# Kernel tuning notes

Measured on AMD Instinct MI355X. Metric: run time of the kernel, lower is better.

The kernel has to match this reference:

```python
import jax, jax.numpy as jnp
import numpy as np

NUM_HEADS = 8
NUM_GROUPS = 32
EPS = 1e-5


def group_norm(x, gamma, beta):
    b, c, h, w = x.shape
    xg = x.reshape(b, NUM_GROUPS, c // NUM_GROUPS, h, w)
    mean = jnp.mean(xg, axis=(2, 3, 4), keepdims=True)
    var = jnp.var(xg, axis=(2, 3, 4), keepdims=True)
    xn = ((xg - mean) * jax.lax.rsqrt(var + EPS)).reshape(b, c, h, w)
    return xn * gamma[None, :, None, None] + beta[None, :, None, None]


def setup_inputs() -> dict:
    key = jax.random.key(0)
    ks = jax.random.split(key, 4)
    b, c, h, w = 16, 512, 32, 32
    x = jax.random.normal(ks[0], (b, c, h, w), dtype=jnp.float32)
    gn_gamma = jnp.ones((c,), dtype=jnp.float32)
    gn_beta = jnp.zeros((c,), dtype=jnp.float32)
    qkv_w = jax.random.normal(ks[1], (3 * c, c), dtype=jnp.float32) * (1.0 / np.sqrt(c))
    qkv_b = jnp.zeros((3 * c,), dtype=jnp.float32)
    proj_w = jax.random.normal(ks[2], (c, c), dtype=jnp.float32) * (1.0 / np.sqrt(c))
    proj_b = jnp.zeros((c,), dtype=jnp.float32)
    return {"x": x, "gn_gamma": gn_gamma, "gn_beta": gn_beta,
            "qkv_w": qkv_w, "qkv_b": qkv_b, "proj_w": proj_w, "proj_b": proj_b}


def reference(x, gn_gamma, gn_beta, qkv_w, qkv_b, proj_w, proj_b):
    b, c, h, w = x.shape
    hd = c // NUM_HEADS
    hw = h * w

    xn = group_norm(x, gn_gamma, gn_beta)
    # 1x1 conv == channel matmul
    qkv = jnp.einsum('oc,bchw->bohw', qkv_w, xn) + qkv_b[None, :, None, None]
    q, k, v = jnp.split(qkv, 3, axis=1)
    q = q.reshape(b, NUM_HEADS, hd, hw)
    k = k.reshape(b, NUM_HEADS, hd, hw)
    v = v.reshape(b, NUM_HEADS, hd, hw)

    scale = 1.0 / np.sqrt(hd)
    attn = jnp.einsum('bhdt,bhds->bhts', q, k) * scale  # [b,H,hw,hw]
    attn = jax.nn.softmax(attn, axis=-1)
    h_attn = jnp.einsum('bhts,bhds->bhdt', attn, v).reshape(b, c, h, w)

    h_attn = jnp.einsum('oc,bchw->bohw', proj_w, h_attn) + proj_b[None, :, None, None]
    return x + h_attn
```

## Files before the change

kernel.cpp:

```cpp
#include <hip/hip_runtime.h>
#include <math.h>

#define NUM_HEADS 8
#define NUM_GROUPS 32
#define EPS 1e-5f

constexpr int B  = 16;
constexpr int C  = 512;
constexpr int HW = 1024;
constexpr int HD = 64;

typedef short bf16x8 __attribute__((ext_vector_type(8)));
typedef float f32x4  __attribute__((ext_vector_type(4)));

#define QSCALE 0.1803368801111f

__device__ inline unsigned short f2bf(float f) {
    union { float f; unsigned int u; } v; v.f = f;
    unsigned int r = (v.u + 0x7FFFu + ((v.u >> 16) & 1u)) >> 16;
    return (unsigned short)r;
}

__device__ __forceinline__ unsigned int pack_trunc(float lo, float hi) {
    return __builtin_amdgcn_perm(__float_as_uint(hi), __float_as_uint(lo), 0x07060302u);
}

__device__ __forceinline__ void gld_lds16(void* lds, const void* g) {
    __builtin_amdgcn_global_load_lds(
        (const __attribute__((address_space(1))) void*)g,
        (__attribute__((address_space(3))) void*)lds, 16, 0, 0);
}

__global__ __launch_bounds__(256)
void groupnorm_t_kernel(const float* __restrict__ x,
                        const float* __restrict__ gamma,
                        const float* __restrict__ beta,
                        unsigned short* __restrict__ xnT) {
    const int bg = blockIdx.x;
    const int b = bg >> 5, g = bg & 31;
    const size_t base = ((size_t)b * C + (size_t)g * 16) * HW;

    float v[4][16];
    float sum = 0.f, sumsq = 0.f;
    #pragma unroll
    for (int p = 0; p < 4; ++p) {
        const int t = threadIdx.x + p * 256;
        #pragma unroll
        for (int cl = 0; cl < 16; ++cl) {
            const float f = x[base + (size_t)cl * HW + t];
            v[p][cl] = f;
            sum += f;
            sumsq += f * f;
        }
    }
    #pragma unroll
    for (int off = 32; off > 0; off >>= 1) {
        sum   += __shfl_down(sum, off, 64);
        sumsq += __shfl_down(sumsq, off, 64);
    }
    __shared__ float s_sum[4], s_sq[4];
    const int wid = threadIdx.x >> 6, lane = threadIdx.x & 63;
    if (lane == 0) { s_sum[wid] = sum; s_sq[wid] = sumsq; }
    __syncthreads();
    const float tsum = s_sum[0] + s_sum[1] + s_sum[2] + s_sum[3];
    const float tsq  = s_sq[0] + s_sq[1] + s_sq[2] + s_sq[3];
    const float mean = tsum * (1.0f / 16384.f);
    const float var  = tsq * (1.0f / 16384.f) - mean * mean;
    const float rstd = rsqrtf(var + EPS);

    float ga[16], be[16];
    #pragma unroll
    for (int cl = 0; cl < 16; ++cl) {
        ga[cl] = gamma[g * 16 + cl] * rstd;
        be[cl] = beta[g * 16 + cl] - mean * ga[cl];
    }

    #pragma unroll
    for (int p = 0; p < 4; ++p) {
        const int t = threadIdx.x + p * 256;
        unsigned short pk[16];
        #pragma unroll
        for (int cl = 0; cl < 16; ++cl)
            pk[cl] = f2bf(v[p][cl] * ga[cl] + be[cl]);
        unsigned short* dst = xnT + ((size_t)(b * 1024 + t)) * 512 + g * 16;
        *(uint4*)dst = *(const uint4*)pk;
        *(uint4*)(dst + 8) = *(const uint4*)(pk + 8);
    }
}

__global__ __launch_bounds__(256)
void wconv_kernel(const float* __restrict__ qkv_w,
                  const float* __restrict__ proj_w,
                  unsigned short* __restrict__ wqb) {
    const int i = blockIdx.x * 256 + threadIdx.x;
    const int n1 = 786432 / 4;
    const int nt = 1048576 / 4;
    if (i >= nt) return;
    const float4 v = (i < n1) ? ((const float4*)qkv_w)[i]
                              : ((const float4*)proj_w)[i - n1];
    ushort4 r;
    r.x = f2bf(v.x); r.y = f2bf(v.y); r.z = f2bf(v.z); r.w = f2bf(v.w);
    ((ushort4*)wqb)[i] = r;
}

__device__ __forceinline__ void mfma_gemm_core(const char* __restrict__ Ab,
                                               const char* __restrict__ Bb,
                                               unsigned short* As,
                                               unsigned short* Bs,
                                               f32x4 acc[4][4]) {
    const int tid = threadIdx.x;
    const int w = tid >> 6, lane = tid & 63;
    const int lo = lane & 15, q4 = lane >> 4;
    const int wm = w >> 1, wn = w & 1;
    const int lrow = lane >> 2, lkc = lane & 3;

    for (int k0 = 0; k0 < 512; k0 += 32) {
        __syncthreads();
        #pragma unroll
        for (int i = 0; i < 2; ++i) {
            const int row = w * 32 + i * 16 + lrow;
            const int kc = lkc ^ ((row >> 1) & 3);
            const size_t goff = (size_t)row * 1024 + k0 * 2 + kc * 16;
            gld_lds16((char*)As + w * 2048 + i * 1024, Ab + goff);
            gld_lds16((char*)Bs + w * 2048 + i * 1024, Bb + goff);
        }
        __syncthreads();

        bf16x8 af[4], bfr[4];
        #pragma unroll
        for (int i = 0; i < 4; ++i) {
            const int ra = wm * 64 + i * 16 + lo;
            af[i]  = *(const bf16x8*)(As + ra * 32 + (q4 ^ ((ra >> 1) & 3)) * 8);
            const int rb = wn * 64 + i * 16 + lo;
            bfr[i] = *(const bf16x8*)(Bs + rb * 32 + (q4 ^ ((rb >> 1) & 3)) * 8);
        }
        #pragma unroll
        for (int mi = 0; mi < 4; ++mi)
            #pragma unroll
            for (int ni = 0; ni < 4; ++ni)
                acc[mi][ni] = __builtin_amdgcn_mfma_f32_16x16x32_bf16(
                    af[mi], bfr[ni], acc[mi][ni], 0, 0, 0);
    }
}

__global__ __launch_bounds__(256)
void qkv_mfma_kernel(const unsigned short* __restrict__ wqb,
                     const unsigned short* __restrict__ xnT,
                     const float* __restrict__ qkv_b,
                     unsigned short* __restrict__ Qt,
                     unsigned short* __restrict__ Kt,
                     unsigned short* __restrict__ Vb) {
    __shared__ __align__(16) unsigned short SMEM[8192];
    unsigned short* As = SMEM;
    unsigned short* Bs = SMEM + 4096;
    const int batch = blockIdx.z;
    const int mBase = blockIdx.y * 128, nBase = blockIdx.x * 128;

    f32x4 acc[4][4] = {};
    mfma_gemm_core((const char*)(wqb + (size_t)mBase * 512),
                   (const char*)(xnT + ((size_t)batch * 1024 + nBase) * 512),
                   As, Bs, acc);

    const int tid = threadIdx.x;
    const int w = tid >> 6, lane = tid & 63;
    const int lo = lane & 15, q4 = lane >> 4;
    const int wm = w >> 1, wn = w & 1;
    const int mw = mBase + wm * 64;
    const int tb = nBase + wn * 64;

    __syncthreads();

    if (mw < 1024) {
        const bool isQ = mw < 512;
        const int head = (mw >> 6) & 7;
        unsigned short* dst = (isQ ? Qt : Kt) + (((size_t)batch * 8 + head) << 16);
        const float sc = isQ ? QSCALE : 1.0f;
        #pragma unroll
        for (int mi = 0; mi < 4; ++mi) {
            const float4 bq = *(const float4*)(qkv_b + mw + mi * 16 + q4 * 4);
            #pragma unroll
            for (int ni = 0; ni < 4; ++ni) {
                const int t = tb + ni * 16 + lo;
                ushort4 pk;
                pk.x = f2bf((acc[mi][ni][0] + bq.x) * sc);
                pk.y = f2bf((acc[mi][ni][1] + bq.y) * sc);
                pk.z = f2bf((acc[mi][ni][2] + bq.z) * sc);
                pk.w = f2bf((acc[mi][ni][3] + bq.w) * sc);
                *(ushort4*)(dst + (size_t)t * 64 + mi * 16 + q4 * 4) = pk;
            }
        }
    } else {
        unsigned short* T = SMEM + w * 2048;
        unsigned short* Vrow = Vb + (size_t)batch * 524288 + (size_t)(mw - 1024) * 1024 + tb;
        const int rl8 = lane >> 3, c8 = lane & 7;
        #pragma unroll
        for (int p = 0; p < 2; ++p) {
            #pragma unroll
            for (int mi2 = 0; mi2 < 2; ++mi2) {
                const int mi = 2 * p + mi2;
                const float4 bq = *(const float4*)(qkv_b + mw + mi * 16 + q4 * 4);
                const int dl = mi2 * 16 + q4 * 4;
                #pragma unroll
                for (int ni = 0; ni < 4; ++ni) {
                    const int tl = ni * 16 + lo;
                    T[(dl + 0) * 64 + tl] = f2bf(acc[mi][ni][0] + bq.x);
                    T[(dl + 1) * 64 + tl] = f2bf(acc[mi][ni][1] + bq.y);
                    T[(dl + 2) * 64 + tl] = f2bf(acc[mi][ni][2] + bq.z);
                    T[(dl + 3) * 64 + tl] = f2bf(acc[mi][ni][3] + bq.w);
                }
            }
            #pragma unroll
            for (int i = 0; i < 4; ++i) {
                const int dl = i * 8 + rl8;
                const uint4 val = *(const uint4*)&T[dl * 64 + c8 * 8];
                *(uint4*)(Vrow + (size_t)(p * 32 + dl) * 1024 + c8 * 8) = val;
            }
        }
    }
}

__global__ __launch_bounds__(256, 4)
void attn_mfma_kernel(const unsigned short* __restrict__ Qt,
                      const unsigned short* __restrict__ Kt,
                      const unsigned short* __restrict__ Vb,
                      unsigned short* __restrict__ attnT) {
    const int bh = blockIdx.x;
    const int b = bh >> 3, h = bh & 7;
    const int tBase = blockIdx.y * 128;
    const int tid = threadIdx.x;
    const int w = tid >> 6, lane = tid & 63;
    const int lo = lane & 15, q4 = lane >> 4;
    const int xr = lo & 7;

    __shared__ __align__(16) unsigned short Ks[64 * 64];
    __shared__ __align__(16) unsigned short Vs[64 * 64];
    __shared__ __align__(16) unsigned short Ps[4 * 2048];

    const unsigned short* Kp = Kt + ((size_t)bh << 16);
    const unsigned short* Vp = Vb + ((size_t)b * 512 + h * 64) * 1024;

    bf16x8 qf[2][2];
    {
        const unsigned short* Qp = Qt + ((size_t)bh * 1024 + tBase + 32 * w) * 64;
        #pragma unroll
        for (int nt = 0; nt < 2; ++nt) {
            qf[nt][0] = *(const bf16x8*)(Qp + (size_t)(16 * nt + lo) * 64 + 8 * q4);
            qf[nt][1] = *(const bf16x8*)(Qp + (size_t)(16 * nt + lo) * 64 + 32 + 8 * q4);
        }
    }

    const int rl = lane >> 3, p8 = lane & 7;
    auto stage = [&](int s0) {
        #pragma unroll
        for (int cc = 0; cc < 2; ++cc) {
            const int r = 16 * w + 8 * cc + rl;
            const int jj = p8 ^ (r & 7);
            gld_lds16(Ks + (16 * w + 8 * cc) * 64, Kp + (size_t)(s0 + r) * 64 + jj * 8);
            gld_lds16(Vs + (16 * w + 8 * cc) * 64, Vp + (size_t)r * 1024 + s0 + jj * 8);
        }
    };

    f32x4 oacc[4][2] = {};
    float lrun[2] = {0.f, 0.f};
    unsigned short* Pw = Ps + w * 2048;

    for (int i = 0; i < 16; ++i) {
        if (i) __syncthreads();
        stage(i * 64);
        __syncthreads();

        f32x4 sacc[4][2] = {};
        #pragma unroll
        for (int mt = 0; mt < 4; ++mt) {
            const unsigned short* kr = Ks + (16 * mt + lo) * 64;
            const bf16x8 a0 = *(const bf16x8*)(kr + ((q4    ) ^ xr) * 8);
            const bf16x8 a1 = *(const bf16x8*)(kr + ((q4 + 4) ^ xr) * 8);
            #pragma unroll
            for (int nt = 0; nt < 2; ++nt) {
                sacc[mt][nt] = __builtin_amdgcn_mfma_f32_16x16x32_bf16(a0, qf[nt][0], sacc[mt][nt], 0, 0, 0);
                sacc[mt][nt] = __builtin_amdgcn_mfma_f32_16x16x32_bf16(a1, qf[nt][1], sacc[mt][nt], 0, 0, 0);
            }
        }

        #pragma unroll
        for (int nt = 0; nt < 2; ++nt) {
            const int t = 16 * nt + lo;
            float ps = 0.f;
            #pragma unroll
            for (int mt = 0; mt < 4; ++mt) {
                const f32x4 s = sacc[mt][nt];
                const float p0 = exp2f(s[0]);
                const float p1 = exp2f(s[1]);
                const float p2 = exp2f(s[2]);
                const float p3 = exp2f(s[3]);
                ps += (p0 + p1) + (p2 + p3);
                uint2 pk;
                pk.x = pack_trunc(p0, p1);
                pk.y = pack_trunc(p2, p3);
                const int sc = 2 * mt + (q4 >> 1);
                *(uint2*)(Pw + t * 64 + ((sc ^ xr) * 8) + 4 * (q4 & 1)) = pk;
            }
            lrun[nt] += ps;
        }

        bf16x8 bp[2][2];
        #pragma unroll
        for (int nt = 0; nt < 2; ++nt) {
            const unsigned short* pr = Pw + (16 * nt + lo) * 64;
            bp[nt][0] = *(const bf16x8*)(pr + ((q4    ) ^ xr) * 8);
            bp[nt][1] = *(const bf16x8*)(pr + ((q4 + 4) ^ xr) * 8);
        }
        #pragma unroll
        for (int md = 0; md < 4; ++md) {
            const unsigned short* vr = Vs + (16 * md + lo) * 64;
            const bf16x8 v0 = *(const bf16x8*)(vr + ((q4    ) ^ xr) * 8);
            const bf16x8 v1 = *(const bf16x8*)(vr + ((q4 + 4) ^ xr) * 8);
            #pragma unroll
            for (int nt = 0; nt < 2; ++nt) {
                oacc[md][nt] = __builtin_amdgcn_mfma_f32_16x16x32_bf16(v0, bp[nt][0], oacc[md][nt], 0, 0, 0);
                oacc[md][nt] = __builtin_amdgcn_mfma_f32_16x16x32_bf16(v1, bp[nt][1], oacc[md][nt], 0, 0, 0);
            }
        }
    }

    #pragma unroll
    for (int nt = 0; nt < 2; ++nt) {
        float lt = lrun[nt];
        lt += __shfl_xor(lt, 16, 64);
        lt += __shfl_xor(lt, 32, 64);
        const float inv = 1.0f / lt;
        const int t = tBase + 32 * w + 16 * nt + lo;
        unsigned short* op = attnT + ((size_t)(b * 1024 + t)) * 512 + h * 64;
        #pragma unroll
        for (int md = 0; md < 4; ++md) {
            uint2 pk;
            pk.x = pack_trunc(oacc[md][nt][0] * inv, oacc[md][nt][1] * inv);
            pk.y = pack_trunc(oacc[md][nt][2] * inv, oacc[md][nt][3] * inv);
            *(uint2*)(op + 16 * md + 4 * q4) = pk;
        }
    }
}

__global__ __launch_bounds__(256)
void proj_mfma_kernel(const unsigned short* __restrict__ wpb,
                      const unsigned short* __restrict__ attnT,
                      const float* __restrict__ proj_b,
                      const float* __restrict__ x,
                      float* __restrict__ out) {
    __shared__ __align__(16) unsigned short As[128 * 32];
    __shared__ __align__(16) unsigned short Bs[128 * 32];
    const int batch = blockIdx.z;
    const int mBase = blockIdx.y * 128, nBase = blockIdx.x * 128;

    f32x4 acc[4][4] = {};
    mfma_gemm_core((const char*)(wpb + (size_t)mBase * 512),
                   (const char*)(attnT + ((size_t)batch * 1024 + nBase) * 512),
                   As, Bs, acc);

    const int tid = threadIdx.x;
    const int w = tid >> 6, lane = tid & 63;
    const int lo = lane & 15, q4 = lane >> 4;
    const int wm = w >> 1, wn = w & 1;
    const float* xb = x + (size_t)batch * 524288;
    float* ob = out + (size_t)batch * 524288;

    #pragma unroll
    for (int mi = 0; mi < 4; ++mi) {
        const int m0 = mBase + wm * 64 + mi * 16 + q4 * 4;
        const float4 bq = *(const float4*)(proj_b + m0);
        #pragma unroll
        for (int ni = 0; ni < 4; ++ni) {
            const int t = nBase + wn * 64 + ni * 16 + lo;
            const size_t o0 = (size_t)m0 * 1024 + t;
            ob[o0]          = acc[mi][ni][0] + bq.x + xb[o0];
            ob[o0 + 1024]   = acc[mi][ni][1] + bq.y + xb[o0 + 1024];
            ob[o0 + 2048]   = acc[mi][ni][2] + bq.z + xb[o0 + 2048];
            ob[o0 + 3072]   = acc[mi][ni][3] + bq.w + xb[o0 + 3072];
        }
    }
}

extern "C" void kernel_launch(void* const* d_in, const int* in_sizes, int n_in,
                              void* d_out, int out_size, void* d_ws, size_t ws_size,
                              hipStream_t stream) {
    const float* x        = (const float*)d_in[0];
    const float* gn_gamma = (const float*)d_in[1];
    const float* gn_beta  = (const float*)d_in[2];
    const float* qkv_w    = (const float*)d_in[3];
    const float* qkv_b    = (const float*)d_in[4];
    const float* proj_w   = (const float*)d_in[5];
    const float* proj_b   = (const float*)d_in[6];
    float* out = (float*)d_out;

    char* wsc = (char*)d_ws;
    unsigned short* xnT   = (unsigned short*)(wsc);
    unsigned short* Qt    = (unsigned short*)(wsc + 16777216);
    unsigned short* Kt    = (unsigned short*)(wsc + 33554432);
    unsigned short* Vb    = (unsigned short*)(wsc + 50331648);
    unsigned short* attnT = (unsigned short*)(wsc + 67108864);
    unsigned short* wqb   = (unsigned short*)(wsc + 83886080);
    unsigned short* wpb   = wqb + 786432;

    groupnorm_t_kernel<<<B * NUM_GROUPS, 256, 0, stream>>>(x, gn_gamma, gn_beta, xnT);

    wconv_kernel<<<1024, 256, 0, stream>>>(qkv_w, proj_w, wqb);

    {
        dim3 grid(HW / 128, (3 * C) / 128, B);
        qkv_mfma_kernel<<<grid, 256, 0, stream>>>(wqb, xnT, qkv_b, Qt, Kt, Vb);
    }

    {
        dim3 grid(B * NUM_HEADS, HW / 128);
        attn_mfma_kernel<<<grid, 256, 0, stream>>>(Qt, Kt, Vb, attnT);
    }

    {
        dim3 grid(HW / 128, C / 128, B);
        proj_mfma_kernel<<<grid, 256, 0, stream>>>(wpb, attnT, proj_b, x, out);
    }
}
```

Before: 223.8 us.

## Double-buffer K/V tiles, permlane-shuffle P in registers, add MFMA priority hints

Splits the K and V shared tiles into two buffers so the next tile's global-to-LDS load is issued while the current tile is being computed, with one barrier per iteration. The P matrix no longer round-trips through shared memory: it is moved into the B-operand layout for the second MFMA with v_permlane32/16_swap. s_setprio raises wave priority around the MFMA blocks. Shared memory use stays roughly the same, and correctness depends on the permlane swap producing exactly the layout the old LDS write and read did.

```diff
diff --git a/kernel.cpp b/kernel.cpp
--- a/kernel.cpp
+++ b/kernel.cpp
@@ -29,6 +29,23 @@
     __builtin_amdgcn_global_load_lds(
         (const __attribute__((address_space(1))) void*)g,
         (__attribute__((address_space(3))) void*)lds, 16, 0, 0);
+}
+
+__device__ __forceinline__ void pl32_swap(unsigned int& a, unsigned int& b) {
+#if __has_builtin(__builtin_amdgcn_permlane32_swap)
+    auto r = __builtin_amdgcn_permlane32_swap(a, b, false, false);
+    a = r[0]; b = r[1];
+#else
+    asm volatile("v_permlane32_swap_b32 %0, %1" : "+v"(a), "+v"(b));
+#endif
+}
+__device__ __forceinline__ void pl16_swap(unsigned int& a, unsigned int& b) {
+#if __has_builtin(__builtin_amdgcn_permlane16_swap)
+    auto r = __builtin_amdgcn_permlane16_swap(a, b, false, false);
+    a = r[0]; b = r[1];
+#else
+    asm volatile("v_permlane16_swap_b32 %0, %1" : "+v"(a), "+v"(b));
+#endif
 }
 
 __global__ __launch_bounds__(256)
@@ -232,9 +249,8 @@
     const int lo = lane & 15, q4 = lane >> 4;
     const int xr = lo & 7;
 
-    __shared__ __align__(16) unsigned short Ks[64 * 64];
-    __shared__ __align__(16) unsigned short Vs[64 * 64];
-    __shared__ __align__(16) unsigned short Ps[4 * 2048];
+    __shared__ __align__(16) unsigned short Ks[2][64 * 64];
+    __shared__ __align__(16) unsigned short Vs[2][64 * 64];
 
     const unsigned short* Kp = Kt + ((size_t)bh << 16);
     const unsigned short* Vp = Vb + ((size_t)b * 512 + h * 64) * 1024;
@@ -250,29 +266,34 @@
     }
 
     const int rl = lane >> 3, p8 = lane & 7;
-    auto stage = [&](int s0) {
+    auto stage = [&](int s0, int bsel) {
         #pragma unroll
         for (int cc = 0; cc < 2; ++cc) {
             const int r = 16 * w + 8 * cc + rl;
             const int jj = p8 ^ (r & 7);
-            gld_lds16(Ks + (16 * w + 8 * cc) * 64, Kp + (size_t)(s0 + r) * 64 + jj * 8);
-            gld_lds16(Vs + (16 * w + 8 * cc) * 64, Vp + (size_t)r * 1024 + s0 + jj * 8);
+            gld_lds16(&Ks[bsel][(16 * w + 8 * cc) * 64], Kp + (size_t)(s0 + r) * 64 + jj * 8);
+            gld_lds16(&Vs[bsel][(16 * w + 8 * cc) * 64], Vp + (size_t)r * 1024 + s0 + jj * 8);
         }
     };
 
     f32x4 oacc[4][2] = {};
     float lrun[2] = {0.f, 0.f};
-    unsigned short* Pw = Ps + w * 2048;
+
+    stage(0, 0);
 
     for (int i = 0; i < 16; ++i) {
-        if (i) __syncthreads();
-        stage(i * 64);
+        const int cur = i & 1;
         __syncthreads();
+        if (i < 15) stage((i + 1) * 64, cur ^ 1);
+
+        const unsigned short* Kc = Ks[cur];
+        const unsigned short* Vc = Vs[cur];
 
         f32x4 sacc[4][2] = {};
+        __builtin_amdgcn_s_setprio(1);
         #pragma unroll
         for (int mt = 0; mt < 4; ++mt) {
-            const unsigned short* kr = Ks + (16 * mt + lo) * 64;
+            const unsigned short* kr = Kc + (16 * mt + lo) * 64;
             const bf16x8 a0 = *(const bf16x8*)(kr + ((q4    ) ^ xr) * 8);
             const bf16x8 a1 = *(const bf16x8*)(kr + ((q4 + 4) ^ xr) * 8);
             #pragma unroll
@@ -281,10 +302,12 @@
                 sacc[mt][nt] = __builtin_amdgcn_mfma_f32_16x16x32_bf16(a1, qf[nt][1], sacc[mt][nt], 0, 0, 0);
             }
         }
-
+        __builtin_amdgcn_s_setprio(0);
+
+        bf16x8 bp[2][2];
         #pragma unroll
         for (int nt = 0; nt < 2; ++nt) {
-            const int t = 16 * nt + lo;
+            unsigned int X[4][2];
             float ps = 0.f;
             #pragma unroll
             for (int mt = 0; mt < 4; ++mt) {
@@ -294,25 +317,35 @@
                 const float p2 = exp2f(s[2]);
                 const float p3 = exp2f(s[3]);
                 ps += (p0 + p1) + (p2 + p3);
-                uint2 pk;
-                pk.x = pack_trunc(p0, p1);
-                pk.y = pack_trunc(p2, p3);
-                const int sc = 2 * mt + (q4 >> 1);
-                *(uint2*)(Pw + t * 64 + ((sc ^ xr) * 8) + 4 * (q4 & 1)) = pk;
+                X[mt][0] = pack_trunc(p0, p1);
+                X[mt][1] = pack_trunc(p2, p3);
             }
             lrun[nt] += ps;
-        }
-
-        bf16x8 bp[2][2];
-        #pragma unroll
-        for (int nt = 0; nt < 2; ++nt) {
-            const unsigned short* pr = Pw + (16 * nt + lo) * 64;
-            bp[nt][0] = *(const bf16x8*)(pr + ((q4    ) ^ xr) * 8);
-            bp[nt][1] = *(const bf16x8*)(pr + ((q4 + 4) ^ xr) * 8);
-        }
+            #pragma unroll
+            for (int h2 = 0; h2 < 2; ++h2) {
+                unsigned int Y0, Y1, Y2, Y3;
+                {
+                    unsigned int a = X[2 * h2][0], bb = X[2 * h2 + 1][0];
+                    pl32_swap(a, bb);
+                    pl16_swap(a, bb);
+                    Y0 = a; Y2 = bb;
+                }
+                {
+                    unsigned int a = X[2 * h2][1], bb = X[2 * h2 + 1][1];
+                    pl32_swap(a, bb);
+                    pl16_swap(a, bb);
+                    Y1 = a; Y3 = bb;
+                }
+                union { unsigned int u[4]; bf16x8 v; } cv;
+                cv.u[0] = Y0; cv.u[1] = Y1; cv.u[2] = Y2; cv.u[3] = Y3;
+                bp[nt][h2] = cv.v;
+            }
+        }
+
+        __builtin_amdgcn_s_setprio(1);
         #pragma unroll
         for (int md = 0; md < 4; ++md) {
-            const unsigned short* vr = Vs + (16 * md + lo) * 64;
+            const unsigned short* vr = Vc + (16 * md + lo) * 64;
             const bf16x8 v0 = *(const bf16x8*)(vr + ((q4    ) ^ xr) * 8);
             const bf16x8 v1 = *(const bf16x8*)(vr + ((q4 + 4) ^ xr) * 8);
             #pragma unroll
@@ -321,6 +354,7 @@
                 oacc[md][nt] = __builtin_amdgcn_mfma_f32_16x16x32_bf16(v1, bp[nt][1], oacc[md][nt], 0, 0, 0);
             }
         }
+        __builtin_amdgcn_s_setprio(0);
     }
 
     #pragma unroll
```

After: 225.9 us. Within noise of the previous version (+0.9%).
